# Performance work log

Hardware: AMD Instinct MI355X
Metric: run time of the kernel (lower is better)

Reference implementation:

```python
import jax, jax.numpy as jnp
import numpy as np

B, N = 2, 131072          # batch, expanded node slots (divisible by flag_size)
FEAT = 69                 # org(3) + pos(3) + uids(63)
KERNELS = 128
FLAG_SIZE = 4             # 1 << dims, dims = 2
BINS = 16                 # 1 << flag_size


def _conv1d(x, w, b, stride=1, padding='SAME'):
    # keras Conv1D: x [B,N,Cin], w [K,Cin,Cout], relu activation
    y = jax.lax.conv_general_dilated(x, w, (stride,), padding,
                                     dimension_numbers=('NWC', 'WIO', 'NWC'))
    return jax.nn.relu(y + b)


def setup_inputs() -> dict:
    key = jax.random.key(0)
    ks = jax.random.split(key, 12)

    def g(k, shape):
        fan_in = int(np.prod(shape[:-1]))
        return (jax.random.normal(k, shape, jnp.float32) / np.sqrt(fan_in)).astype(jnp.float32)

    c_x = FEAT + KERNELS                 # 197 after each pre conv concat
    c_flags = 2 * FEAT + KERNELS         # 266 flags-head input
    c_sym = c_flags + FLAG_SIZE          # 270 symbols-branch input

    return {
        'inputs': jax.random.normal(ks[0], (B, N, FEAT), jnp.float32),
        'w_pre0': g(ks[1], (3, FEAT, KERNELS)),   'b_pre0': jnp.zeros((KERNELS,), jnp.float32),
        'w_pre1': g(ks[2], (3, c_x, KERNELS)),    'b_pre1': jnp.zeros((KERNELS,), jnp.float32),
        'w_flags': g(ks[3], (c_flags, FLAG_SIZE)), 'b_flags': jnp.zeros((FLAG_SIZE,), jnp.float32),
        'w_merge': g(ks[4], (FLAG_SIZE, c_sym, KERNELS)), 'b_merge': jnp.zeros((KERNELS,), jnp.float32),
        'w_post0': g(ks[5], (3, KERNELS, KERNELS)), 'b_post0': jnp.zeros((KERNELS,), jnp.float32),
        'w_post1': g(ks[6], (3, KERNELS, KERNELS)), 'b_post1': jnp.zeros((KERNELS,), jnp.float32),
        'w_post2': g(ks[7], (3, KERNELS, KERNELS)), 'b_post2': jnp.zeros((KERNELS,), jnp.float32),
        'w_post3': g(ks[8], (3, KERNELS, KERNELS)), 'b_post3': jnp.zeros((KERNELS,), jnp.float32),
        'w_sym': g(ks[9], (KERNELS, BINS)),        'b_sym': jnp.zeros((BINS,), jnp.float32),
    }


def _forward(inputs, w_pre0, b_pre0, w_pre1, b_pre1, w_flags, b_flags,
             w_merge, b_merge, w_post0, b_post0, w_post1, b_post1,
             w_post2, b_post2, w_post3, b_post3, w_sym, b_sym):
    # pos offsets = (3, 6); pos = inputs[..., 3:5] (2 columns)
    pos = inputs[..., 3:5]
    sort = jnp.argsort(pos, axis=-2)                       # [B, N, 2]
    # gather with batch_dims=1 along node axis
    X = jnp.take_along_axis(inputs, sort[..., 1:2], axis=1)   # sorted by pos col 1
    x0 = jax.lax.stop_gradient(X)                            # [B, N, 69]
    X = jnp.concatenate([x0, _conv1d(X, w_pre0, b_pre0)], axis=-1)  # [B, N, 197]
    X = jnp.concatenate([x0, _conv1d(X, w_pre1, b_pre1)], axis=-1)  # [B, N, 197]
    X = jnp.concatenate([X, jnp.take_along_axis(inputs, sort[..., 0:1], axis=1)], axis=-1)  # [B, N, 266]

    F = jax.nn.sigmoid(X @ w_flags + b_flags)               # [B, N, 4]

    S = jax.lax.stop_gradient(jnp.concatenate([F, X], axis=-1))     # [B, N, 270]
    S = _conv1d(S, w_merge, b_merge, stride=FLAG_SIZE, padding='VALID')  # [B, N/4, 128]
    for w, b in ((w_post0, b_post0), (w_post1, b_post1), (w_post2, b_post2), (w_post3, b_post3)):
        S = _conv1d(S, w, b)
    S = jax.nn.softmax(S @ w_sym + b_sym, axis=-1)          # [B, N/4, 16]

    Fd = (F[..., 0] - F[..., 1]).reshape(F.shape[0], -1, FLAG_SIZE)  # [B, N/4, 4]
    return jnp.concatenate([Fd, S], axis=-1)                # [B, N/4, 20]


def reference(inputs, w_pre0, b_pre0, w_pre1, b_pre1, w_flags, b_flags,
              w_merge, b_merge, w_post0, b_post0, w_post1, b_post1,
              w_post2, b_post2, w_post3, b_post3, w_sym, b_sym):
    return _forward(inputs, w_pre0, b_pre0, w_pre1, b_pre1, w_flags, b_flags,
                    w_merge, b_merge, w_post0, b_post0, w_post1, b_post1,
                    w_post2, b_post2, w_post3, b_post3, w_sym, b_sym)
```

## Files before the change

### kernel.cpp

```cpp
#include <hip/hip_runtime.h>
#include <hip/hip_bf16.h>
#include <math.h>

#define NPOS 131072
#define NF   69
#define NMRG 32768
#define TILE 2048
#define TPS  64
#define NSORT 4
#define EPT  16
#define XCW  288

typedef __attribute__((ext_vector_type(8))) short short8;
typedef __attribute__((ext_vector_type(4))) short s16x4;
typedef __bf16 bf16x8 __attribute__((ext_vector_type(8)));
typedef __attribute__((ext_vector_type(4))) float f32x4;

static __device__ inline bf16x8 as_bf16x8(short8 v){ union{short8 s; bf16x8 b;} u; u.s=v; return u.b; }
static __device__ inline short f2bf(float x){ __hip_bfloat16 h = __float2bfloat16(x); return *(short*)&h; }
static __device__ inline float bf2f(short s){ return __uint_as_float(((unsigned)(unsigned short)s)<<16); }

static __device__ inline void gld16(const short* g, short* l){
  __builtin_amdgcn_global_load_lds(
      (const __attribute__((address_space(1))) unsigned int*)g,
      (__attribute__((address_space(3))) unsigned int*)l, 16, 0, 0);
}

__global__ void k_make_keys(const float* __restrict__ inp, unsigned* __restrict__ kA,
                            unsigned* __restrict__ vA){
  unsigned t = blockIdx.x*256u + threadIdx.x;
  unsigned s = t >> 17, i = t & (NPOS-1u);
  unsigned b = s >> 1, ch = 3u + (s & 1u);
  float x = inp[((size_t)b*NPOS + i)*NF + ch];
  unsigned u = __float_as_uint(x);
  u = (u & 0x80000000u) ? ~u : (u | 0x80000000u);
  kA[t] = u; vA[t] = i;
}

__global__ __launch_bounds__(256) void k_hist(const unsigned* __restrict__ src,
                                              unsigned* __restrict__ hist, int shift){
  __shared__ unsigned h[256];
  int tid = threadIdx.x;
  h[tid] = 0u; __syncthreads();
  int s = blockIdx.x / TPS, tile = blockIdx.x % TPS;
  const unsigned* ks = src + (size_t)s*NPOS + (size_t)tile*TILE;
  for (int r = 0; r < TILE/256; ++r){
    unsigned d = (ks[r*256 + tid] >> shift) & 255u;
    atomicAdd(&h[d], 1u);
  }
  __syncthreads();
  hist[s*16384 + tid*TPS + tile] = h[tid];
}

__global__ __launch_bounds__(256) void k_scan(unsigned* __restrict__ hist){
  __shared__ unsigned tot[256];
  int tid = threadIdx.x; int s = blockIdx.x;
  unsigned* g = hist + s*16384;
  unsigned sum = 0;
  for (int q = 0; q < TPS; ++q) sum += g[tid*TPS + q];
  tot[tid] = sum;
  __syncthreads();
  if (tid == 0){
    unsigned run = 0;
    for (int t = 0; t < 256; ++t){ unsigned tmp = tot[t]; tot[t] = run; run += tmp; }
  }
  __syncthreads();
  unsigned run = tot[tid];
  for (int q = 0; q < TPS; ++q){ unsigned tmp = g[tid*TPS+q]; g[tid*TPS+q] = run; run += tmp; }
}

__global__ __launch_bounds__(128) void k_scatter(const unsigned* __restrict__ srcK,
    const unsigned* __restrict__ srcV, unsigned* __restrict__ dstK, unsigned* __restrict__ dstV,
    const unsigned* __restrict__ off, int shift){
  __shared__ unsigned short cnt[256*128];
  int tid = threadIdx.x;
  unsigned* cz = (unsigned*)cnt;
  for (int idx = tid; idx < 256*128/2; idx += 128) cz[idx] = 0u;
  __syncthreads();
  int s = blockIdx.x / TPS, tile = blockIdx.x % TPS;
  const unsigned* ks = srcK + (size_t)s*NPOS + (size_t)tile*TILE;
  const unsigned* vs = srcV + (size_t)s*NPOS + (size_t)tile*TILE;
  unsigned k8[EPT], v8[EPT];
  #pragma unroll
  for (int r = 0; r < EPT; ++r){
    k8[r] = ks[tid*EPT + r];
    v8[r] = vs[tid*EPT + r];
    unsigned d = (k8[r] >> shift) & 255u;
    cnt[d*128 + tid]++;
  }
  __syncthreads();
  for (int dd = 0; dd < 2; ++dd){
    int d = tid + dd*128;
    unsigned run = 0;
    for (int t = 0; t < 128; ++t){ unsigned tmp = cnt[d*128 + t]; cnt[d*128 + t] = (unsigned short)run; run += tmp; }
  }
  __syncthreads();
  const unsigned* ob = off + s*16384;
  #pragma unroll
  for (int r = 0; r < EPT; ++r){
    unsigned d = (k8[r] >> shift) & 255u;
    unsigned rk = cnt[d*128 + tid];
    cnt[d*128 + tid] = (unsigned short)(rk + 1u);
    unsigned pos = ob[d*TPS + tile] + rk;
    dstK[(size_t)s*NPOS + pos] = k8[r];
    dstV[(size_t)s*NPOS + pos] = v8[r];
  }
}

__global__ __launch_bounds__(256) void k_cvt(const float* __restrict__ inp,
                                             short* __restrict__ inpb, int b){
  int t = blockIdx.x*256 + threadIdx.x;
  int i = t/9, q = t - i*9;
  const float* sp = inp + ((size_t)b*NPOS + i)*NF + q*8;
  short o[8];
  #pragma unroll
  for (int e = 0; e < 8; ++e){
    int c = q*8 + e;
    o[e] = (c < NF) ? f2bf(sp[e]) : (short)0;
  }
  *(short8*)(inpb + (size_t)i*72 + q*8) = *(short8*)o;
}

__global__ __launch_bounds__(256) void k_gath2(const short* __restrict__ inpb,
    const unsigned* __restrict__ P1, const unsigned* __restrict__ P0,
    short* __restrict__ XA, short* __restrict__ Xcat){
  int t = blockIdx.x*256 + threadIdx.x;
  int i = t/18, u = t - i*18;
  int p = u/9, q = u - p*9;
  if (p){
    short8 v = *(const short8*)(inpb + (size_t)P1[i]*72 + q*8);
    *(short8*)(XA + (size_t)i*224 + 128 + q*8) = v;
    s16x4 lo = {v[0],v[1],v[2],v[3]}, hi = {v[4],v[5],v[6],v[7]};
    *(s16x4*)(Xcat + (size_t)i*XCW + 132 + q*8) = lo;
    *(s16x4*)(Xcat + (size_t)i*XCW + 136 + q*8) = hi;
  } else {
    short8 v = *(const short8*)(inpb + (size_t)P0[i]*72 + q*8);
    *(short8*)(Xcat + (size_t)i*XCW + 208 + q*8) = v;
    if (q == 8){
      s16x4 z4 = {0,0,0,0};
      *(s16x4*)(Xcat + (size_t)i*XCW + 204) = z4;
      short8 z8 = {0,0,0,0,0,0,0,0};
      *(short8*)(Xcat + (size_t)i*XCW + 280) = z8;
    }
  }
}

static __device__ inline void prep_one(const float* __restrict__ w, short* __restrict__ out,
                                       int t, int KC, int NQ, int mode){
  int lane = t & 63, ni = (t>>6) & 1, ksub = (t>>7) & 1;
  int rest = t >> 8;
  int q = rest % NQ;
  int wv = rest / NQ;
  int tap = q / KC, cc = q - tap*KC;
  int nn = wv*32 + ni*16 + (lane & 15);
  int chb = cc*64 + ksub*32 + ((lane >> 4) & 3)*8;
  short o[8];
  #pragma unroll
  for (int e = 0; e < 8; ++e){
    int ch = chb + e;
    float val = 0.f;
    if (mode == 0){ if (ch < 69)  val = w[((size_t)tap*69  + ch)*128 + nn]; }
    else if (mode == 1){
      if (ch < 128)      val = w[((size_t)tap*197 + 69 + ch)*128 + nn];
      else if (ch < 197) val = w[((size_t)tap*197 + ch - 128)*128 + nn];
    }
    else if (mode == 2){ if (ch < 128) val = w[((size_t)tap*128 + ch)*128 + nn]; }
    else {
      int tm = ch / XCW, cm = ch - tm*XCW;
      int orig = -1;
      if (cm < 128)                     orig = 73 + cm;
      else if (cm < 201)                orig = cm - 128;
      else if (cm >= 208 && cm < 277)   orig = cm - 7;
      if (orig >= 0) val = w[((size_t)tm*270 + orig)*128 + nn];
    }
    o[e] = f2bf(val);
  }
  *(short8*)(out + (size_t)t*8) = *(short8*)o;
}

__global__ __launch_bounds__(256) void k_prepAll(
    const float* __restrict__ w_pre0, const float* __restrict__ w_pre1,
    const float* __restrict__ q0w, const float* __restrict__ q1w,
    const float* __restrict__ q2w, const float* __restrict__ q3w,
    const float* __restrict__ w_merge, const float* __restrict__ w_flags,
    short* o0, short* o1, short* oq0, short* oq1, short* oq2, short* oq3,
    short* om, float* owf){
  int t = blockIdx.x*256 + threadIdx.x;
  if (t < 6144)        prep_one(w_pre0, o0,  t,        2,  6,  0);
  else if (t < 18432)  prep_one(w_pre1, o1,  t-6144,   4,  12, 1);
  else if (t < 24576)  prep_one(q0w,    oq0, t-18432,  2,  6,  2);
  else if (t < 30720)  prep_one(q1w,    oq1, t-24576,  2,  6,  2);
  else if (t < 36864)  prep_one(q2w,    oq2, t-30720,  2,  6,  2);
  else if (t < 43008)  prep_one(q3w,    oq3, t-36864,  2,  6,  2);
  else if (t < 61440)  prep_one(w_merge,om,  t-43008,  18, 18, 3);
  else if (t < 62592){
    int t2 = t - 61440;
    int c = t2 >> 2, q = t2 & 3;
    float v = 0.f;
    if (c < 128)                  v = w_flags[(69 + c)*4 + q];
    else if (c >= 132 && c < 201) v = w_flags[(c - 132)*4 + q];
    else if (c >= 208 && c < 277) v = w_flags[(197 + c - 208)*4 + q];
    owf[t2] = v;
  }
}

#define OSTR2 136

template<int CPAD, int MT, int FUSE>
__global__ __launch_bounds__(256) void k_conv3s(
    const short* __restrict__ src, int sstride, int coff, int cin,
    const short* __restrict__ wB, const float* __restrict__ bias,
    short* __restrict__ dst, int dstride, int n,
    const float* __restrict__ ex1, const float* __restrict__ ex2,
    float* __restrict__ ex3, const float* __restrict__ ex4)
{
  constexpr int KC  = CPAD/64;
  constexpr int KH  = CPAD/2;
  constexpr int KC2 = KH/64;
  constexpr int SPH = 3*KC2*2;
  constexpr int NST = 2*SPH;
  constexpr int PF  = 4;
  constexpr int ASTR = KH + 8;
  constexpr int AG  = KH/8;
  constexpr int MI  = MT/16;
  constexpr size_t ABYTES = (size_t)(MT+2)*ASTR*2;
  constexpr size_t OBYTES = (size_t)MT*OSTR2*2;
  constexpr size_t LBYTES = (ABYTES > OBYTES) ? ABYTES : OBYTES;
  __shared__ __attribute__((aligned(16))) char LDS[LBYTES];
  short* A_s = (short*)LDS;
  short* OTs = (short*)LDS;
  int tid = threadIdx.x;
  int i0 = blockIdx.x*MT;
  int wv = tid >> 6, lane = tid & 63;
  int lm = lane & 15, lk = lane >> 4;

  const short* wBw = wB + (size_t)wv*(KC*6)*1024 + (size_t)lane*8;
  auto LB = [&](int ls, int ni){
    int h = ls / SPH, r1 = ls % SPH;
    int tp = r1 / (KC2*2), r2 = r1 % (KC2*2);
    int c = r2 >> 1, ksub = r2 & 1;
    int q = tp*KC + h*KC2 + c;
    return as_bf16x8(*(const short8*)(wBw + ((q*2 + ksub)*2 + ni)*512));
  };
  auto stageA = [&](int h){
    for (int idx = tid; idx < (MT+2)*AG; idx += 256){
      int r = idx / AG, g = idx - r*AG;
      int pos = i0 - 1 + r;
      int cb = h*KH + g*8;
      short8 v = {0,0,0,0,0,0,0,0};
      if (pos >= 0 && pos < n && cb < cin){
        const short* sp = src + (size_t)pos*sstride + coff + cb;
        if (cb + 8 <= cin) v = *(const short8*)sp;
        else { for (int j = 0; cb + j < cin; ++j) v[j] = sp[j]; }
      }
      *(short8*)(A_s + r*ASTR + g*8) = v;
    }
  };

  bf16x8 bq[PF][2];
  #pragma unroll
  for (int s = 0; s < PF; ++s){ bq[s][0] = LB(s,0); bq[s][1] = LB(s,1); }
  stageA(0);
  __syncthreads();

  f32x4 acc[MI][2] = {};
  #pragma unroll
  for (int ls = 0; ls < NST; ++ls){
    if (ls == SPH){
      __syncthreads();
      stageA(1);
      __syncthreads();
    }
    int slot = ls % PF;
    bf16x8 b0 = bq[slot][0], b1 = bq[slot][1];
    if (ls + PF < NST){ bq[slot][0] = LB(ls+PF,0); bq[slot][1] = LB(ls+PF,1); }
    int r1 = ls % SPH;
    int tp = r1 / (KC2*2), r2 = r1 % (KC2*2);
    int c = r2 >> 1, ksub = r2 & 1;
    bf16x8 a[MI];
    #pragma unroll
    for (int mi = 0; mi < MI; ++mi)
      a[mi] = as_bf16x8(*(const short8*)(A_s + (mi*16+lm+tp)*ASTR + c*64 + ksub*32 + lk*8));
    #pragma unroll
    for (int mi = 0; mi < MI; ++mi){
      acc[mi][0] = __builtin_amdgcn_mfma_f32_16x16x32_bf16(a[mi], b0, acc[mi][0], 0, 0, 0);
      acc[mi][1] = __builtin_amdgcn_mfma_f32_16x16x32_bf16(a[mi], b1, acc[mi][1], 0, 0, 0);
    }
  }
  __syncthreads();
  float b0s = bias[wv*32 + lm], b1s = bias[wv*32 + 16 + lm];
  #pragma unroll
  for (int mi = 0; mi < MI; ++mi)
    #pragma unroll
    for (int ni = 0; ni < 2; ++ni){
      float bb = ni ? b1s : b0s;
      #pragma unroll
      for (int r = 0; r < 4; ++r)
        OTs[(mi*16 + lk*4 + r)*OSTR2 + wv*32 + ni*16 + lm] = f2bf(fmaxf(acc[mi][ni][r] + bb, 0.f));
    }
  __syncthreads();

  if constexpr (FUSE != 2){
    constexpr int CPT = (MT*128/8)/256;
    int unit0 = tid*CPT;
    int r = unit0 >> 4, uq = unit0 & 15;
    const short* row = OTs + r*OSTR2 + uq*8;
    short* dp = dst + (size_t)(i0 + r)*dstride + uq*8;
    #pragma unroll
    for (int j = 0; j < CPT; ++j)
      *(short8*)(dp + j*8) = *(const short8*)(row + j*8);
  }

  if constexpr (FUSE == 2){
    int row = tid >> 3, part = tid & 7;
    const short* srow = OTs + row*OSTR2 + part*16;
    float l[16];
    #pragma unroll
    for (int t2 = 0; t2 < 16; ++t2) l[t2] = (part == 0) ? ex2[t2] : 0.f;
    #pragma unroll
    for (int g = 0; g < 2; ++g){
      short8 x8 = *(const short8*)(srow + g*8);
      #pragma unroll
      for (int e = 0; e < 8; ++e){
        float x = bf2f(x8[e]);
        const float* w = ex1 + (part*16 + g*8 + e)*16;
        #pragma unroll
        for (int t2 = 0; t2 < 16; ++t2) l[t2] = fmaf(x, w[t2], l[t2]);
      }
    }
    #pragma unroll
    for (int m = 1; m < 8; m <<= 1)
      #pragma unroll
      for (int t2 = 0; t2 < 16; ++t2) l[t2] += __shfl_xor(l[t2], m);
    if (part == 0){
      float mx = l[0];
      #pragma unroll
      for (int t2 = 1; t2 < 16; ++t2) mx = fmaxf(mx, l[t2]);
      float sum = 0.f;
      #pragma unroll
      for (int t2 = 0; t2 < 16; ++t2){ l[t2] = expf(l[t2]-mx); sum += l[t2]; }
      float inv = 1.f/sum;
      size_t j = (size_t)(i0 + row);
      float* o = ex3 + j*20;
      #pragma unroll
      for (int k2 = 0; k2 < 4; ++k2){
        size_t r4 = (size_t)(4*j + k2)*4;
        o[k2] = ex4[r4] - ex4[r4+1];
      }
      #pragma unroll
      for (int t2 = 0; t2 < 16; ++t2) o[4+t2] = l[t2]*inv;
    }
  }
}

__global__ __launch_bounds__(256) void k_flags2(short* __restrict__ Xcat,
    const float* __restrict__ Wf2, const float* __restrict__ bf, float* __restrict__ F){
  size_t i = (size_t)blockIdx.x*256 + threadIdx.x;
  const short* x = Xcat + i*XCW;
  float a0 = bf[0], a1 = bf[1], a2 = bf[2], a3 = bf[3];
  for (int g = 0; g < XCW/8; ++g){
    short8 x8 = *(const short8*)(x + g*8);
    #pragma unroll
    for (int e = 0; e < 8; ++e){
      float xv = bf2f(x8[e]);
      const float* w = Wf2 + (g*8+e)*4;
      a0 = fmaf(xv,w[0],a0); a1 = fmaf(xv,w[1],a1); a2 = fmaf(xv,w[2],a2); a3 = fmaf(xv,w[3],a3);
    }
  }
  float f0 = 1.f/(1.f+expf(-a0)), f1 = 1.f/(1.f+expf(-a1));
  float f2 = 1.f/(1.f+expf(-a2)), f3 = 1.f/(1.f+expf(-a3));
  float* f = F + i*4;
  f[0]=f0; f[1]=f1; f[2]=f2; f[3]=f3;
  short* xc = Xcat + i*XCW + 128;
  xc[0]=f2bf(f0); xc[1]=f2bf(f1); xc[2]=f2bf(f2); xc[3]=f2bf(f3);
}

__global__ __launch_bounds__(256) void k_mergem4(const short* __restrict__ Xf,
    const short* __restrict__ wB, const float* __restrict__ bias, short* __restrict__ dst)
{
  constexpr int NS = 4*XCW/64;
  constexpr size_t ABYTES = 2*2048*2;
  constexpr size_t OBYTES = (size_t)32*OSTR2*2;
  constexpr size_t LBYTES = (ABYTES > OBYTES) ? ABYTES : OBYTES;
  __shared__ __attribute__((aligned(16))) char LDS[LBYTES];
  short* A_s = (short*)LDS;
  short* OTs = (short*)LDS;
  int tid = threadIdx.x;
  int j0 = blockIdx.x*32;
  int wv = tid >> 6, lane = tid & 63;
  int lm = lane & 15, lk = lane >> 4;
  auto stageA = [&](int s){
    int r = tid >> 3, kv = tid & 7;
    const short* gp = Xf + (size_t)(j0 + r)*(4*XCW) + s*64 + ((kv ^ (r&7))*8);
    gld16(gp, A_s + (s&1)*2048 + tid*8);
  };
  const short* wBl = wB + (size_t)wv*NS*2048 + (size_t)lane*8;
  auto LB = [&](int s, int ks, int ni){
    return as_bf16x8(*(const short8*)(wBl + ((size_t)(s*2 + ks)*2 + ni)*512));
  };
  bf16x8 c00 = LB(0,0,0), c01 = LB(0,0,1), c10 = LB(0,1,0), c11 = LB(0,1,1);
  stageA(0);
  __syncthreads();
  f32x4 acc[2][2] = {};
  for (int s = 0; s < NS; ++s){
    bf16x8 n00, n01, n10, n11;
    if (s < NS-1){
      n00 = LB(s+1,0,0); n01 = LB(s+1,0,1); n10 = LB(s+1,1,0); n11 = LB(s+1,1,1);
      stageA(s+1);
    }
    const short* Ab = A_s + (s&1)*2048;
    bf16x8 a[2];
    #pragma unroll
    for (int mi = 0; mi < 2; ++mi){
      int r = mi*16 + lm;
      a[mi] = as_bf16x8(*(const short8*)(Ab + r*64 + ((lk ^ (r&7))*8)));
    }
    #pragma unroll
    for (int mi = 0; mi < 2; ++mi){
      acc[mi][0] = __builtin_amdgcn_mfma_f32_16x16x32_bf16(a[mi], c00, acc[mi][0], 0, 0, 0);
      acc[mi][1] = __builtin_amdgcn_mfma_f32_16x16x32_bf16(a[mi], c01, acc[mi][1], 0, 0, 0);
    }
    #pragma unroll
    for (int mi = 0; mi < 2; ++mi){
      int r = mi*16 + lm;
      a[mi] = as_bf16x8(*(const short8*)(Ab + r*64 + (((4+lk) ^ (r&7))*8)));
    }
    #pragma unroll
    for (int mi = 0; mi < 2; ++mi){
      acc[mi][0] = __builtin_amdgcn_mfma_f32_16x16x32_bf16(a[mi], c10, acc[mi][0], 0, 0, 0);
      acc[mi][1] = __builtin_amdgcn_mfma_f32_16x16x32_bf16(a[mi], c11, acc[mi][1], 0, 0, 0);
    }
    __syncthreads();
    c00 = n00; c01 = n01; c10 = n10; c11 = n11;
  }
  float b0 = bias[wv*32 + lm], b1 = bias[wv*32 + 16 + lm];
  #pragma unroll
  for (int mi = 0; mi < 2; ++mi)
    #pragma unroll
    for (int ni = 0; ni < 2; ++ni){
      float bb = ni ? b1 : b0;
      #pragma unroll
      for (int r = 0; r < 4; ++r)
        OTs[(mi*16 + lk*4 + r)*OSTR2 + wv*32 + ni*16 + lm] = f2bf(fmaxf(acc[mi][ni][r] + bb, 0.f));
    }
  __syncthreads();
  {
    int unit0 = tid*2;
    int r = unit0 >> 4, uq = unit0 & 15;
    const short* row = OTs + r*OSTR2 + uq*8;
    short* dp = dst + (size_t)(j0 + r)*128 + uq*8;
    #pragma unroll
    for (int j = 0; j < 2; ++j)
      *(short8*)(dp + j*8) = *(const short8*)(row + j*8);
  }
}

extern "C" void kernel_launch(void* const* d_in, const int* in_sizes, int n_in,
                              void* d_out, int out_size, void* d_ws, size_t ws_size,
                              hipStream_t stream){
  const float* inp     = (const float*)d_in[0];
  const float* w_pre0  = (const float*)d_in[1];
  const float* b_pre0  = (const float*)d_in[2];
  const float* w_pre1  = (const float*)d_in[3];
  const float* b_pre1  = (const float*)d_in[4];
  const float* w_flags = (const float*)d_in[5];
  const float* b_flags = (const float*)d_in[6];
  const float* w_merge = (const float*)d_in[7];
  const float* b_merge = (const float*)d_in[8];
  const float* w_post[4] = {(const float*)d_in[9], (const float*)d_in[11],
                            (const float*)d_in[13], (const float*)d_in[15]};
  const float* b_post[4] = {(const float*)d_in[10], (const float*)d_in[12],
                            (const float*)d_in[14], (const float*)d_in[16]};
  const float* w_sym   = (const float*)d_in[17];
  const float* b_sym   = (const float*)d_in[18];
  float* outp = (float*)d_out;

  char* p = (char*)d_ws;
  unsigned* kA = (unsigned*)p; p += (size_t)NSORT*NPOS*4;
  unsigned* vA = (unsigned*)p; p += (size_t)NSORT*NPOS*4;
  unsigned* kB = (unsigned*)p; p += (size_t)NSORT*NPOS*4;
  unsigned* vB = (unsigned*)p; p += (size_t)NSORT*NPOS*4;
  unsigned* hist = (unsigned*)p; p += (size_t)NSORT*16384*4;
  short* inpb = (short*)p; p += (size_t)NPOS*72*2;
  short* XA   = (short*)p; p += (size_t)NPOS*224*2;
  short* Xcat = (short*)p; p += (size_t)NPOS*XCW*2;
  float* Fbuf = (float*)p; p += (size_t)NPOS*4*4;
  short* M0   = (short*)p; p += (size_t)NMRG*128*2;
  short* M1   = (short*)p; p += (size_t)NMRG*128*2;
  short* wb0  = (short*)p; p += (size_t)3*2*8192*2;
  short* wb1  = (short*)p; p += (size_t)3*4*8192*2;
  short* wbq0 = (short*)p; p += (size_t)3*2*8192*2;
  short* wbq1 = (short*)p; p += (size_t)3*2*8192*2;
  short* wbq2 = (short*)p; p += (size_t)3*2*8192*2;
  short* wbq3 = (short*)p; p += (size_t)3*2*8192*2;
  short* wbm  = (short*)p; p += (size_t)18*8192*2;
  float* wf2  = (float*)p; p += (size_t)XCW*4*4;
  if ((size_t)(p - (char*)d_ws) > ws_size) return;
  short* wbq[4] = {wbq0, wbq1, wbq2, wbq3};

  k_prepAll<<<(62592+255)/256, 256, 0, stream>>>(
      w_pre0, w_pre1, w_post[0], w_post[1], w_post[2], w_post[3], w_merge, w_flags,
      wb0, wb1, wbq0, wbq1, wbq2, wbq3, wbm, wf2);

  k_make_keys<<<NSORT*NPOS/256, 256, 0, stream>>>(inp, kA, vA);
  unsigned *sk = kA, *sv = vA, *dk = kB, *dv = vB;
  for (int pass = 0; pass < 4; ++pass){
    int shift = pass*8;
    k_hist<<<NSORT*TPS, 256, 0, stream>>>(sk, hist, shift);
    k_scan<<<NSORT, 256, 0, stream>>>(hist);
    k_scatter<<<NSORT*TPS, 128, 0, stream>>>(sk, sv, dk, dv, hist, shift);
    unsigned* t;
    t = sk; sk = dk; dk = t;
    t = sv; sv = dv; dv = t;
  }
  for (int b = 0; b < 2; ++b){
    const unsigned* P0 = sv + (size_t)(b*2+0)*NPOS;
    const unsigned* P1 = sv + (size_t)(b*2+1)*NPOS;
    k_cvt<<<NPOS*9/256, 256, 0, stream>>>(inp, inpb, b);
    k_gath2<<<NPOS*18/256, 256, 0, stream>>>(inpb, P1, P0, XA, Xcat);
    k_conv3s<128,64,0><<<NPOS/64, 256, 0, stream>>>(XA, 224, 128, 69, wb0, b_pre0, XA, 224, NPOS,
                                                    nullptr, nullptr, nullptr, nullptr);
    k_conv3s<256,64,0><<<NPOS/64, 256, 0, stream>>>(XA, 224, 0, 197, wb1, b_pre1, Xcat, XCW, NPOS,
                                                    nullptr, nullptr, nullptr, nullptr);
    k_flags2<<<NPOS/256, 256, 0, stream>>>(Xcat, wf2, b_flags, Fbuf);
    k_mergem4<<<NMRG/32, 256, 0, stream>>>(Xcat, wbm, b_merge, M0);
    k_conv3s<128,32,0><<<NMRG/32, 256, 0, stream>>>(M0, 128, 0, 128, wbq[0], b_post[0], M1, 128, NMRG,
                                                    nullptr, nullptr, nullptr, nullptr);
    k_conv3s<128,32,0><<<NMRG/32, 256, 0, stream>>>(M1, 128, 0, 128, wbq[1], b_post[1], M0, 128, NMRG,
                                                    nullptr, nullptr, nullptr, nullptr);
    k_conv3s<128,32,0><<<NMRG/32, 256, 0, stream>>>(M0, 128, 0, 128, wbq[2], b_post[2], M1, 128, NMRG,
                                                    nullptr, nullptr, nullptr, nullptr);
    k_conv3s<128,32,2><<<NMRG/32, 256, 0, stream>>>(M1, 128, 0, 128, wbq[3], b_post[3], M0, 128, NMRG,
                                                    w_sym, b_sym, outp + (size_t)b*NMRG*20, Fbuf);
  }
}
```

Baseline: 599.3 us.

## Process both batches in a single launch per stage with per-batch buffers

Instead of looping over the batch on the host and launching every stage once per batch element, each kernel now derives the batch index from blockIdx and runs over both batch elements in one grid, provided the workspace can hold two copies of the intermediate buffers. This halves the number of kernel launches and doubles the grid size, which fills the GPU better in the small post-merge convolutions that had only 1024 blocks. The cost is twice the intermediate workspace, and it falls back to one batch per launch if the workspace is too small.

```diff
diff --git a/kernel.cpp b/kernel.cpp
--- a/kernel.cpp
+++ b/kernel.cpp
@@ -10,6 +10,13 @@
 #define NSORT 4
 #define EPT  16
 #define XCW  288
+
+#define INB_B ((size_t)NPOS*72)
+#define XA_B  ((size_t)NPOS*224)
+#define XC_B  ((size_t)NPOS*XCW)
+#define F_B   ((size_t)NPOS*4)
+#define M_B   ((size_t)NMRG*128)
+#define OUT_B ((size_t)NMRG*20)
 
 typedef __attribute__((ext_vector_type(8))) short short8;
 typedef __attribute__((ext_vector_type(4))) short s16x4;
@@ -108,8 +115,9 @@
 }
 
 __global__ __launch_bounds__(256) void k_cvt(const float* __restrict__ inp,
-                                             short* __restrict__ inpb, int b){
-  int t = blockIdx.x*256 + threadIdx.x;
+                                             short* __restrict__ inpb){
+  int b = blockIdx.x / 4608;
+  int t = (blockIdx.x - b*4608)*256 + threadIdx.x;
   int i = t/9, q = t - i*9;
   const float* sp = inp + ((size_t)b*NPOS + i)*NF + q*8;
   short o[8];
@@ -118,29 +126,35 @@
     int c = q*8 + e;
     o[e] = (c < NF) ? f2bf(sp[e]) : (short)0;
   }
-  *(short8*)(inpb + (size_t)i*72 + q*8) = *(short8*)o;
+  *(short8*)(inpb + (size_t)b*INB_B + (size_t)i*72 + q*8) = *(short8*)o;
 }
 
 __global__ __launch_bounds__(256) void k_gath2(const short* __restrict__ inpb,
-    const unsigned* __restrict__ P1, const unsigned* __restrict__ P0,
+    const unsigned* __restrict__ svb,
     short* __restrict__ XA, short* __restrict__ Xcat){
-  int t = blockIdx.x*256 + threadIdx.x;
+  int b = blockIdx.x / 9216;
+  int t = (blockIdx.x - b*9216)*256 + threadIdx.x;
   int i = t/18, u = t - i*18;
   int p = u/9, q = u - p*9;
+  const unsigned* P0 = svb + (size_t)(b*2+0)*NPOS;
+  const unsigned* P1 = svb + (size_t)(b*2+1)*NPOS;
+  const short* ib = inpb + (size_t)b*INB_B;
+  short* xa = XA + (size_t)b*XA_B;
+  short* xc = Xcat + (size_t)b*XC_B;
   if (p){
-    short8 v = *(const short8*)(inpb + (size_t)P1[i]*72 + q*8);
-    *(short8*)(XA + (size_t)i*224 + 128 + q*8) = v;
+    short8 v = *(const short8*)(ib + (size_t)P1[i]*72 + q*8);
+    *(short8*)(xa + (size_t)i*224 + 128 + q*8) = v;
     s16x4 lo = {v[0],v[1],v[2],v[3]}, hi = {v[4],v[5],v[6],v[7]};
-    *(s16x4*)(Xcat + (size_t)i*XCW + 132 + q*8) = lo;
-    *(s16x4*)(Xcat + (size_t)i*XCW + 136 + q*8) = hi;
+    *(s16x4*)(xc + (size_t)i*XCW + 132 + q*8) = lo;
+    *(s16x4*)(xc + (size_t)i*XCW + 136 + q*8) = hi;
   } else {
-    short8 v = *(const short8*)(inpb + (size_t)P0[i]*72 + q*8);
-    *(short8*)(Xcat + (size_t)i*XCW + 208 + q*8) = v;
+    short8 v = *(const short8*)(ib + (size_t)P0[i]*72 + q*8);
+    *(short8*)(xc + (size_t)i*XCW + 208 + q*8) = v;
     if (q == 8){
       s16x4 z4 = {0,0,0,0};
-      *(s16x4*)(Xcat + (size_t)i*XCW + 204) = z4;
+      *(s16x4*)(xc + (size_t)i*XCW + 204) = z4;
       short8 z8 = {0,0,0,0,0,0,0,0};
-      *(short8*)(Xcat + (size_t)i*XCW + 280) = z8;
+      *(short8*)(xc + (size_t)i*XCW + 280) = z8;
     }
   }
 }
@@ -210,9 +224,10 @@
 __global__ __launch_bounds__(256) void k_conv3s(
     const short* __restrict__ src, int sstride, int coff, int cin,
     const short* __restrict__ wB, const float* __restrict__ bias,
-    short* __restrict__ dst, int dstride, int n,
+    short* __restrict__ dst, int dstride, int n, int bpb,
     const float* __restrict__ ex1, const float* __restrict__ ex2,
-    float* __restrict__ ex3, const float* __restrict__ ex4)
+    float* __restrict__ ex3, const float* __restrict__ ex4,
+    size_t sB, size_t dB)
 {
   constexpr int KC  = CPAD/64;
   constexpr int KH  = CPAD/2;
@@ -230,7 +245,10 @@
   short* A_s = (short*)LDS;
   short* OTs = (short*)LDS;
   int tid = threadIdx.x;
-  int i0 = blockIdx.x*MT;
+  int b  = blockIdx.x / bpb;
+  int i0 = (blockIdx.x - b*bpb)*MT;
+  const short* srcb = src + (size_t)b*sB;
+  short* dstb = dst + (size_t)b*dB;
   int wv = tid >> 6, lane = tid & 63;
   int lm = lane & 15, lk = lane >> 4;
 
@@ -249,7 +267,7 @@
       int cb = h*KH + g*8;
       short8 v = {0,0,0,0,0,0,0,0};
       if (pos >= 0 && pos < n && cb < cin){
-        const short* sp = src + (size_t)pos*sstride + coff + cb;
+        const short* sp = srcb + (size_t)pos*sstride + coff + cb;
         if (cb + 8 <= cin) v = *(const short8*)sp;
         else { for (int j = 0; cb + j < cin; ++j) v[j] = sp[j]; }
       }
@@ -305,7 +323,7 @@
     int unit0 = tid*CPT;
     int r = unit0 >> 4, uq = unit0 & 15;
     const short* row = OTs + r*OSTR2 + uq*8;
-    short* dp = dst + (size_t)(i0 + r)*dstride + uq*8;
+    short* dp = dstb + (size_t)(i0 + r)*dstride + uq*8;
     #pragma unroll
     for (int j = 0; j < CPT; ++j)
       *(short8*)(dp + j*8) = *(const short8*)(row + j*8);
@@ -314,6 +332,8 @@
   if constexpr (FUSE == 2){
     int row = tid >> 3, part = tid & 7;
     const short* srow = OTs + row*OSTR2 + part*16;
+    const float* ex4b = ex4 + (size_t)b*F_B;
+    float* ex3b = ex3 + (size_t)b*OUT_B;
     float l[16];
     #pragma unroll
     for (int t2 = 0; t2 < 16; ++t2) l[t2] = (part == 0) ? ex2[t2] : 0.f;
@@ -341,11 +361,11 @@
       for (int t2 = 0; t2 < 16; ++t2){ l[t2] = expf(l[t2]-mx); sum += l[t2]; }
       float inv = 1.f/sum;
       size_t j = (size_t)(i0 + row);
-      float* o = ex3 + j*20;
+      float* o = ex3b + j*20;
       #pragma unroll
       for (int k2 = 0; k2 < 4; ++k2){
         size_t r4 = (size_t)(4*j + k2)*4;
-        o[k2] = ex4[r4] - ex4[r4+1];
+        o[k2] = ex4b[r4] - ex4b[r4+1];
       }
       #pragma unroll
       for (int t2 = 0; t2 < 16; ++t2) o[4+t2] = l[t2]*inv;
@@ -355,8 +375,10 @@
 
 __global__ __launch_bounds__(256) void k_flags2(short* __restrict__ Xcat,
     const float* __restrict__ Wf2, const float* __restrict__ bf, float* __restrict__ F){
-  size_t i = (size_t)blockIdx.x*256 + threadIdx.x;
-  const short* x = Xcat + i*XCW;
+  int b = blockIdx.x >> 9;
+  size_t i = (size_t)(blockIdx.x & 511)*256 + threadIdx.x;
+  short* xb = Xcat + (size_t)b*XC_B;
+  const short* x = xb + i*XCW;
   float a0 = bf[0], a1 = bf[1], a2 = bf[2], a3 = bf[3];
   for (int g = 0; g < XCW/8; ++g){
     short8 x8 = *(const short8*)(x + g*8);
@@ -369,15 +391,14 @@
   }
   float f0 = 1.f/(1.f+expf(-a0)), f1 = 1.f/(1.f+expf(-a1));
   float f2 = 1.f/(1.f+expf(-a2)), f3 = 1.f/(1.f+expf(-a3));
-  float* f = F + i*4;
+  float* f = F + (size_t)b*F_B + i*4;
   f[0]=f0; f[1]=f1; f[2]=f2; f[3]=f3;
-  short* xc = Xcat + i*XCW + 128;
+  short* xc = xb + i*XCW + 128;
   xc[0]=f2bf(f0); xc[1]=f2bf(f1); xc[2]=f2bf(f2); xc[3]=f2bf(f3);
 }
 
 __global__ __launch_bounds__(256) void k_mergem4(const short* __restrict__ Xf,
-    const short* __restrict__ wB, const float* __restrict__ bias, short* __restrict__ dst)
-{
+    const short* __restrict__ wB, const float* __restrict__ bias, short* __restrict__ dst){
   constexpr int NS = 4*XCW/64;
   constexpr size_t ABYTES = 2*2048*2;
   constexpr size_t OBYTES = (size_t)32*OSTR2*2;
@@ -386,12 +407,15 @@
   short* A_s = (short*)LDS;
   short* OTs = (short*)LDS;
   int tid = threadIdx.x;
-  int j0 = blockIdx.x*32;
+  int b  = blockIdx.x >> 10;
+  int j0 = (blockIdx.x & 1023)*32;
+  const short* Xfb = Xf + (size_t)b*XC_B;
+  short* dstb = dst + (size_t)b*M_B;
   int wv = tid >> 6, lane = tid & 63;
   int lm = lane & 15, lk = lane >> 4;
   auto stageA = [&](int s){
     int r = tid >> 3, kv = tid & 7;
-    const short* gp = Xf + (size_t)(j0 + r)*(4*XCW) + s*64 + ((kv ^ (r&7))*8);
+    const short* gp = Xfb + (size_t)(j0 + r)*(4*XCW) + s*64 + ((kv ^ (r&7))*8);
     gld16(gp, A_s + (s&1)*2048 + tid*8);
   };
   const short* wBl = wB + (size_t)wv*NS*2048 + (size_t)lane*8;
@@ -448,7 +472,7 @@
     int unit0 = tid*2;
     int r = unit0 >> 4, uq = unit0 & 15;
     const short* row = OTs + r*OSTR2 + uq*8;
-    short* dp = dst + (size_t)(j0 + r)*128 + uq*8;
+    short* dp = dstb + (size_t)(j0 + r)*128 + uq*8;
     #pragma unroll
     for (int j = 0; j < 2; ++j)
       *(short8*)(dp + j*8) = *(const short8*)(row + j*8);
@@ -481,12 +505,6 @@
   unsigned* kB = (unsigned*)p; p += (size_t)NSORT*NPOS*4;
   unsigned* vB = (unsigned*)p; p += (size_t)NSORT*NPOS*4;
   unsigned* hist = (unsigned*)p; p += (size_t)NSORT*16384*4;
-  short* inpb = (short*)p; p += (size_t)NPOS*72*2;
-  short* XA   = (short*)p; p += (size_t)NPOS*224*2;
-  short* Xcat = (short*)p; p += (size_t)NPOS*XCW*2;
-  float* Fbuf = (float*)p; p += (size_t)NPOS*4*4;
-  short* M0   = (short*)p; p += (size_t)NMRG*128*2;
-  short* M1   = (short*)p; p += (size_t)NMRG*128*2;
   short* wb0  = (short*)p; p += (size_t)3*2*8192*2;
   short* wb1  = (short*)p; p += (size_t)3*4*8192*2;
   short* wbq0 = (short*)p; p += (size_t)3*2*8192*2;
@@ -495,8 +513,19 @@
   short* wbq3 = (short*)p; p += (size_t)3*2*8192*2;
   short* wbm  = (short*)p; p += (size_t)18*8192*2;
   float* wf2  = (float*)p; p += (size_t)XCW*4*4;
+  short* wbq[4] = {wbq0, wbq1, wbq2, wbq3};
+
+  size_t perb = INB_B*2 + XA_B*2 + XC_B*2 + F_B*4 + 2*M_B*2;
+  size_t used = (size_t)(p - (char*)d_ws);
+  int NB = (used + 2*perb <= ws_size) ? 2 : 1;
+
+  short* inpb = (short*)p; p += (size_t)NB*INB_B*2;
+  short* XA   = (short*)p; p += (size_t)NB*XA_B*2;
+  short* Xcat = (short*)p; p += (size_t)NB*XC_B*2;
+  float* Fbuf = (float*)p; p += (size_t)NB*F_B*4;
+  short* M0   = (short*)p; p += (size_t)NB*M_B*2;
+  short* M1   = (short*)p; p += (size_t)NB*M_B*2;
   if ((size_t)(p - (char*)d_ws) > ws_size) return;
-  short* wbq[4] = {wbq0, wbq1, wbq2, wbq3};
 
   k_prepAll<<<(62592+255)/256, 256, 0, stream>>>(
       w_pre0, w_pre1, w_post[0], w_post[1], w_post[2], w_post[3], w_merge, w_flags,
@@ -513,24 +542,25 @@
     t = sk; sk = dk; dk = t;
     t = sv; sv = dv; dv = t;
   }
-  for (int b = 0; b < 2; ++b){
-    const unsigned* P0 = sv + (size_t)(b*2+0)*NPOS;
-    const unsigned* P1 = sv + (size_t)(b*2+1)*NPOS;
-    k_cvt<<<NPOS*9/256, 256, 0, stream>>>(inp, inpb, b);
-    k_gath2<<<NPOS*18/256, 256, 0, stream>>>(inpb, P1, P0, XA, Xcat);
-    k_conv3s<128,64,0><<<NPOS/64, 256, 0, stream>>>(XA, 224, 128, 69, wb0, b_pre0, XA, 224, NPOS,
-                                                    nullptr, nullptr, nullptr, nullptr);
-    k_conv3s<256,64,0><<<NPOS/64, 256, 0, stream>>>(XA, 224, 0, 197, wb1, b_pre1, Xcat, XCW, NPOS,
-                                                    nullptr, nullptr, nullptr, nullptr);
-    k_flags2<<<NPOS/256, 256, 0, stream>>>(Xcat, wf2, b_flags, Fbuf);
-    k_mergem4<<<NMRG/32, 256, 0, stream>>>(Xcat, wbm, b_merge, M0);
-    k_conv3s<128,32,0><<<NMRG/32, 256, 0, stream>>>(M0, 128, 0, 128, wbq[0], b_post[0], M1, 128, NMRG,
-                                                    nullptr, nullptr, nullptr, nullptr);
-    k_conv3s<128,32,0><<<NMRG/32, 256, 0, stream>>>(M1, 128, 0, 128, wbq[1], b_post[1], M0, 128, NMRG,
-                                                    nullptr, nullptr, nullptr, nullptr);
-    k_conv3s<128,32,0><<<NMRG/32, 256, 0, stream>>>(M0, 128, 0, 128, wbq[2], b_post[2], M1, 128, NMRG,
-                                                    nullptr, nullptr, nullptr, nullptr);
-    k_conv3s<128,32,2><<<NMRG/32, 256, 0, stream>>>(M1, 128, 0, 128, wbq[3], b_post[3], M0, 128, NMRG,
-                                                    w_sym, b_sym, outp + (size_t)b*NMRG*20, Fbuf);
-  }
-}
+
+  for (int bb = 0; bb < 2; bb += NB){
+    const float* inpO = inp + (size_t)bb*NPOS*NF;
+    const unsigned* svO = sv + (size_t)bb*2*NPOS;
+    k_cvt<<<NB*4608, 256, 0, stream>>>(inpO, inpb);
+    k_gath2<<<NB*9216, 256, 0, stream>>>(inpb, svO, XA, Xcat);
+    k_conv3s<128,64,0><<<NB*2048, 256, 0, stream>>>(XA, 224, 128, 69, wb0, b_pre0, XA, 224, NPOS,
+        2048, nullptr, nullptr, nullptr, nullptr, XA_B, XA_B);
+    k_conv3s<256,64,0><<<NB*2048, 256, 0, stream>>>(XA, 224, 0, 197, wb1, b_pre1, Xcat, XCW, NPOS,
+        2048, nullptr, nullptr, nullptr, nullptr, XA_B, XC_B);
+    k_flags2<<<NB*512, 256, 0, stream>>>(Xcat, wf2, b_flags, Fbuf);
+    k_mergem4<<<NB*1024, 256, 0, stream>>>(Xcat, wbm, b_merge, M0);
+    k_conv3s<128,32,0><<<NB*1024, 256, 0, stream>>>(M0, 128, 0, 128, wbq[0], b_post[0], M1, 128, NMRG,
+        1024, nullptr, nullptr, nullptr, nullptr, M_B, M_B);
+    k_conv3s<128,32,0><<<NB*1024, 256, 0, stream>>>(M1, 128, 0, 128, wbq[1], b_post[1], M0, 128, NMRG,
+        1024, nullptr, nullptr, nullptr, nullptr, M_B, M_B);
+    k_conv3s<128,32,0><<<NB*1024, 256, 0, stream>>>(M0, 128, 0, 128, wbq[2], b_post[2], M1, 128, NMRG,
+        1024, nullptr, nullptr, nullptr, nullptr, M_B, M_B);
+    k_conv3s<128,32,2><<<NB*1024, 256, 0, stream>>>(M1, 128, 0, 128, wbq[3], b_post[3], M0, 128, NMRG,
+        1024, w_sym, b_sym, outp + (size_t)bb*OUT_B, Fbuf, M_B, M_B);
+  }
+}
```

Result: no change. 603.1 us (+0.6%).

## Fuse merge and post-conv tail into one cooperative kernel with grid syncs

Applied to the files above, without the earlier changes.

Replaces the five back-to-back launches of the tail (strided merge conv, four post convs, softmax head) with one cooperative kernel. It uses grid-wide syncs between phases and a new in-kernel conv routine that stages halo rows in LDS. The aim is to remove the launch gaps and drain/fill between dependent small kernels. The cost is grid barrier overhead and requiring all 1024 blocks to be co-resident. If the cooperative launch fails, it falls back to the original launches.

```diff
diff --git a/kernel.cpp b/kernel.cpp
--- a/kernel.cpp
+++ b/kernel.cpp
@@ -1,6 +1,9 @@
 #include <hip/hip_runtime.h>
 #include <hip/hip_bf16.h>
+#include <hip/hip_cooperative_groups.h>
 #include <math.h>
+
+namespace cg = cooperative_groups;
 
 #define NPOS 131072
 #define NF   69
@@ -10,6 +13,8 @@
 #define NSORT 4
 #define EPT  16
 #define XCW  288
+#define F_B   ((size_t)NPOS*4)
+#define OUT_B ((size_t)NMRG*20)
 
 typedef __attribute__((ext_vector_type(8))) short short8;
 typedef __attribute__((ext_vector_type(4))) short s16x4;
@@ -375,14 +380,10 @@
   xc[0]=f2bf(f0); xc[1]=f2bf(f1); xc[2]=f2bf(f2); xc[3]=f2bf(f3);
 }
 
-__global__ __launch_bounds__(256) void k_mergem4(const short* __restrict__ Xf,
-    const short* __restrict__ wB, const float* __restrict__ bias, short* __restrict__ dst)
-{
+
+static __device__ void merge_ph(char* LDS, const short* __restrict__ Xf,
+    const short* __restrict__ wB, const float* __restrict__ bias, short* __restrict__ dst){
   constexpr int NS = 4*XCW/64;
-  constexpr size_t ABYTES = 2*2048*2;
-  constexpr size_t OBYTES = (size_t)32*OSTR2*2;
-  constexpr size_t LBYTES = (ABYTES > OBYTES) ? ABYTES : OBYTES;
-  __shared__ __attribute__((aligned(16))) char LDS[LBYTES];
   short* A_s = (short*)LDS;
   short* OTs = (short*)LDS;
   int tid = threadIdx.x;
@@ -453,6 +454,152 @@
     for (int j = 0; j < 2; ++j)
       *(short8*)(dp + j*8) = *(const short8*)(row + j*8);
   }
+}
+
+template<int FUSE>
+static __device__ void conv_ph(char* LDS, const short* __restrict__ src,
+    const short* __restrict__ wB, const float* __restrict__ bias, short* __restrict__ dst,
+    const float* ex1, const float* ex2, float* ex3, const float* ex4){
+  constexpr int SPH = 6, NST = 12, PF = 4, ASTR = 72, AG = 8;
+  short* A_s = (short*)LDS;
+  short* OTs = (short*)LDS;
+  int tid = threadIdx.x;
+  int i0 = blockIdx.x*32;
+  int wv = tid >> 6, lane = tid & 63;
+  int lm = lane & 15, lk = lane >> 4;
+  const short* wBw = wB + (size_t)wv*12*1024 + (size_t)lane*8;
+  auto LB = [&](int ls, int ni){
+    int h = ls / SPH, r1 = ls % SPH;
+    int tp = r1 >> 1, ksub = r1 & 1;
+    int q = tp*2 + h;
+    return as_bf16x8(*(const short8*)(wBw + ((q*2 + ksub)*2 + ni)*512));
+  };
+  auto stageA = [&](int h){
+    for (int idx = tid; idx < 34*AG; idx += 256){
+      int r = idx / AG, g = idx - r*AG;
+      int pos = i0 - 1 + r;
+      short8 v = {0,0,0,0,0,0,0,0};
+      if (pos >= 0 && pos < NMRG)
+        v = *(const short8*)(src + (size_t)pos*128 + h*64 + g*8);
+      *(short8*)(A_s + r*ASTR + g*8) = v;
+    }
+  };
+  bf16x8 bq[PF][2];
+  #pragma unroll
+  for (int s = 0; s < PF; ++s){ bq[s][0] = LB(s,0); bq[s][1] = LB(s,1); }
+  stageA(0);
+  __syncthreads();
+  f32x4 acc[2][2] = {};
+  #pragma unroll
+  for (int ls = 0; ls < NST; ++ls){
+    if (ls == SPH){
+      __syncthreads();
+      stageA(1);
+      __syncthreads();
+    }
+    int slot = ls % PF;
+    bf16x8 b0 = bq[slot][0], b1 = bq[slot][1];
+    if (ls + PF < NST){ bq[slot][0] = LB(ls+PF,0); bq[slot][1] = LB(ls+PF,1); }
+    int r1 = ls % SPH;
+    int tp = r1 >> 1, ksub = r1 & 1;
+    bf16x8 a[2];
+    #pragma unroll
+    for (int mi = 0; mi < 2; ++mi)
+      a[mi] = as_bf16x8(*(const short8*)(A_s + (mi*16+lm+tp)*ASTR + ksub*32 + lk*8));
+    #pragma unroll
+    for (int mi = 0; mi < 2; ++mi){
+      acc[mi][0] = __builtin_amdgcn_mfma_f32_16x16x32_bf16(a[mi], b0, acc[mi][0], 0, 0, 0);
+      acc[mi][1] = __builtin_amdgcn_mfma_f32_16x16x32_bf16(a[mi], b1, acc[mi][1], 0, 0, 0);
+    }
+  }
+  __syncthreads();
+  float b0s = bias[wv*32 + lm], b1s = bias[wv*32 + 16 + lm];
+  #pragma unroll
+  for (int mi = 0; mi < 2; ++mi)
+    #pragma unroll
+    for (int ni = 0; ni < 2; ++ni){
+      float bb = ni ? b1s : b0s;
+      #pragma unroll
+      for (int r = 0; r < 4; ++r)
+        OTs[(mi*16 + lk*4 + r)*OSTR2 + wv*32 + ni*16 + lm] = f2bf(fmaxf(acc[mi][ni][r] + bb, 0.f));
+    }
+  __syncthreads();
+  if constexpr (FUSE != 2){
+    int unit0 = tid*2;
+    int r = unit0 >> 4, uq = unit0 & 15;
+    const short* row = OTs + r*OSTR2 + uq*8;
+    short* dp = dst + (size_t)(i0 + r)*128 + uq*8;
+    #pragma unroll
+    for (int j = 0; j < 2; ++j)
+      *(short8*)(dp + j*8) = *(const short8*)(row + j*8);
+  } else {
+    int row = tid >> 3, part = tid & 7;
+    const short* srow = OTs + row*OSTR2 + part*16;
+    float l[16];
+    #pragma unroll
+    for (int t2 = 0; t2 < 16; ++t2) l[t2] = (part == 0) ? ex2[t2] : 0.f;
+    #pragma unroll
+    for (int g = 0; g < 2; ++g){
+      short8 x8 = *(const short8*)(srow + g*8);
+      #pragma unroll
+      for (int e = 0; e < 8; ++e){
+        float x = bf2f(x8[e]);
+        const float* w = ex1 + (part*16 + g*8 + e)*16;
+        #pragma unroll
+        for (int t2 = 0; t2 < 16; ++t2) l[t2] = fmaf(x, w[t2], l[t2]);
+      }
+    }
+    #pragma unroll
+    for (int m = 1; m < 8; m <<= 1)
+      #pragma unroll
+      for (int t2 = 0; t2 < 16; ++t2) l[t2] += __shfl_xor(l[t2], m);
+    if (part == 0){
+      float mx = l[0];
+      #pragma unroll
+      for (int t2 = 1; t2 < 16; ++t2) mx = fmaxf(mx, l[t2]);
+      float sum = 0.f;
+      #pragma unroll
+      for (int t2 = 0; t2 < 16; ++t2){ l[t2] = expf(l[t2]-mx); sum += l[t2]; }
+      float inv = 1.f/sum;
+      size_t j = (size_t)(i0 + row);
+      float* o = ex3 + j*20;
+      #pragma unroll
+      for (int k2 = 0; k2 < 4; ++k2){
+        size_t r4 = (size_t)(4*j + k2)*4;
+        o[k2] = ex4[r4] - ex4[r4+1];
+      }
+      #pragma unroll
+      for (int t2 = 0; t2 < 16; ++t2) o[4+t2] = l[t2]*inv;
+    }
+  }
+}
+
+struct TailA {
+  const short* Xf; const short* wbm; const float* bm;
+  short* M0; short* M1;
+  const short* wq0; const short* wq1; const short* wq2; const short* wq3;
+  const float* bq0; const float* bq1; const float* bq2; const float* bq3;
+  const float* wsym; const float* bsym; float* outp; const float* Fb;
+};
+
+__global__ __launch_bounds__(256) void k_tail(TailA a){
+  __shared__ __attribute__((aligned(16))) char LDS[(size_t)32*OSTR2*2];
+  cg::grid_group grid = cg::this_grid();
+  merge_ph(LDS, a.Xf, a.wbm, a.bm, a.M0);
+  __threadfence(); grid.sync();
+  conv_ph<0>(LDS, a.M0, a.wq0, a.bq0, a.M1, nullptr, nullptr, nullptr, nullptr);
+  __threadfence(); grid.sync();
+  conv_ph<0>(LDS, a.M1, a.wq1, a.bq1, a.M0, nullptr, nullptr, nullptr, nullptr);
+  __threadfence(); grid.sync();
+  conv_ph<0>(LDS, a.M0, a.wq2, a.bq2, a.M1, nullptr, nullptr, nullptr, nullptr);
+  __threadfence(); grid.sync();
+  conv_ph<2>(LDS, a.M1, a.wq3, a.bq3, a.M0, a.wsym, a.bsym, a.outp, a.Fb);
+}
+
+__global__ __launch_bounds__(256) void k_mergem4(const short* __restrict__ Xf,
+    const short* __restrict__ wB, const float* __restrict__ bias, short* __restrict__ dst){
+  __shared__ __attribute__((aligned(16))) char LDS[(size_t)32*OSTR2*2];
+  merge_ph(LDS, Xf, wB, bias, dst);
 }
 
 extern "C" void kernel_launch(void* const* d_in, const int* in_sizes, int n_in,
@@ -523,14 +670,24 @@
     k_conv3s<256,64,0><<<NPOS/64, 256, 0, stream>>>(XA, 224, 0, 197, wb1, b_pre1, Xcat, XCW, NPOS,
                                                     nullptr, nullptr, nullptr, nullptr);
     k_flags2<<<NPOS/256, 256, 0, stream>>>(Xcat, wf2, b_flags, Fbuf);
-    k_mergem4<<<NMRG/32, 256, 0, stream>>>(Xcat, wbm, b_merge, M0);
-    k_conv3s<128,32,0><<<NMRG/32, 256, 0, stream>>>(M0, 128, 0, 128, wbq[0], b_post[0], M1, 128, NMRG,
-                                                    nullptr, nullptr, nullptr, nullptr);
-    k_conv3s<128,32,0><<<NMRG/32, 256, 0, stream>>>(M1, 128, 0, 128, wbq[1], b_post[1], M0, 128, NMRG,
-                                                    nullptr, nullptr, nullptr, nullptr);
-    k_conv3s<128,32,0><<<NMRG/32, 256, 0, stream>>>(M0, 128, 0, 128, wbq[2], b_post[2], M1, 128, NMRG,
-                                                    nullptr, nullptr, nullptr, nullptr);
-    k_conv3s<128,32,2><<<NMRG/32, 256, 0, stream>>>(M1, 128, 0, 128, wbq[3], b_post[3], M0, 128, NMRG,
-                                                    w_sym, b_sym, outp + (size_t)b*NMRG*20, Fbuf);
-  }
-}
+
+    TailA ta = {Xcat, wbm, b_merge, M0, M1,
+                wbq[0], wbq[1], wbq[2], wbq[3],
+                b_post[0], b_post[1], b_post[2], b_post[3],
+                w_sym, b_sym, outp + (size_t)b*OUT_B, Fbuf};
+    void* kargs[] = {&ta};
+    hipError_t err = hipLaunchCooperativeKernel((void*)k_tail, dim3(NMRG/32), dim3(256),
+                                                kargs, 0u, stream);
+    if (err != hipSuccess){
+      k_mergem4<<<NMRG/32, 256, 0, stream>>>(Xcat, wbm, b_merge, M0);
+      k_conv3s<128,32,0><<<NMRG/32, 256, 0, stream>>>(M0, 128, 0, 128, wbq[0], b_post[0], M1, 128, NMRG,
+                                                      nullptr, nullptr, nullptr, nullptr);
+      k_conv3s<128,32,0><<<NMRG/32, 256, 0, stream>>>(M1, 128, 0, 128, wbq[1], b_post[1], M0, 128, NMRG,
+                                                      nullptr, nullptr, nullptr, nullptr);
+      k_conv3s<128,32,0><<<NMRG/32, 256, 0, stream>>>(M0, 128, 0, 128, wbq[2], b_post[2], M1, 128, NMRG,
+                                                      nullptr, nullptr, nullptr, nullptr);
+      k_conv3s<128,32,2><<<NMRG/32, 256, 0, stream>>>(M1, 128, 0, 128, wbq[3], b_post[3], M0, 128, NMRG,
+                                                      w_sym, b_sym, outp + (size_t)b*OUT_B, Fbuf);
+    }
+  }
+}
```

Result: slower. 2.290 ms (+282.1%).
